# Optimization experiments

Measured on AMD Instinct MI355X. Metric: run time of the kernel, lower is better.

## Reference

```python
import jax, jax.numpy as jnp
import numpy as np

B, N, K, C = 8, 4096, 32, 64
RADIUS = 0.15
CIN = C + 3  # dp_fj: concat(dp[3], fj[C])


def _ball_query(p, radius, k):
    """p: (B,N,3). Returns neighbor indices (B,N,K): first k points (in index
    order) within radius of each query, padded with the first valid neighbor
    (ballquery semantics; query point itself is always index 0 candidate)."""
    sq = jnp.sum(p * p, axis=-1)                                  # (B,N)
    d2 = sq[:, :, None] + sq[:, None, :] - 2.0 * jnp.einsum('bnd,bmd->bnm', p, p)
    n = p.shape[1]
    within = d2 <= radius * radius
    key = jnp.where(within, jnp.arange(n, dtype=jnp.int32)[None, None, :], n)
    order = jnp.argsort(key, axis=-1)[..., :k]                    # (B,N,K)
    valid = jnp.take_along_axis(key, order, axis=-1) < n
    first = order[..., :1]
    return jnp.where(valid, order, first)


def _conv2d_1x1(x, w, b):
    # x: (B,Cin,N,K), w: (Cout,Cin), b: (Cout,)
    return jnp.einsum('oi,bink->bonk', w, x) + b[None, :, None, None]


def _conv1d_1x1(x, w, b):
    # x: (B,Cin,N)
    return jnp.einsum('oi,bin->bon', w, x) + b[None, :, None]


def setup_inputs() -> dict:
    key = jax.random.key(0)
    ks = jax.random.split(key, 16)
    s = 0.05
    inp = {
        'p': jax.random.uniform(ks[0], (B, N, 3), dtype=jnp.float32),
        'f': jax.random.normal(ks[1], (B, C, N), dtype=jnp.float32),
        # attn_local: convblock2d (CIN -> C), no act
        'w_attn': jax.random.normal(ks[2], (C, CIN), dtype=jnp.float32) * s,
        'b_attn': jnp.zeros((C,), jnp.float32),
        # convs: convblock2d (CIN -> C, relu) then (C -> C, no act)
        'w1': jax.random.normal(ks[3], (C, CIN), dtype=jnp.float32) * s,
        'b1': jnp.zeros((C,), jnp.float32),
        'w2': jax.random.normal(ks[4], (C, C), dtype=jnp.float32) * s,
        'b2': jnp.zeros((C,), jnp.float32),
        # ffn: convblock1d (C -> C*expansion=C, relu) then (C -> C, no act)
        'wf1': jax.random.normal(ks[5], (C, C), dtype=jnp.float32) * s,
        'bf1': jnp.zeros((C,), jnp.float32),
        'wf2': jax.random.normal(ks[6], (C, C), dtype=jnp.float32) * s,
        'bf2': jnp.zeros((C,), jnp.float32),
    }
    return inp


def reference(p, f, w_attn, b_attn, w1, b1, w2, b2, wf1, bf1, wf2, bf2):
    bidx = jnp.arange(B)[:, None, None]
    idx = _ball_query(p, RADIUS, K)                               # (B,N,K) int
    pj = p[bidx, idx]                                             # (B,N,K,3)
    dp = (pj - p[:, :, None, :]).transpose(0, 3, 1, 2)            # (B,3,N,K)
    ft = f.transpose(0, 2, 1)                                     # (B,N,C)
    fj = ft[bidx, idx].transpose(0, 3, 1, 2)                      # (B,C,N,K)

    fj_cat = jnp.concatenate([dp, fj], axis=1)                    # (B,CIN,N,K)

    attn = _conv2d_1x1(fj_cat, w_attn, b_attn)                    # (B,C,N,K)
    x = jax.nn.relu(_conv2d_1x1(fj_cat, w1, b1))
    x = _conv2d_1x1(x, w2, b2)                                    # (B,C,N,K)

    # new_attention, 4D path: softmax over neighbor axis (tau=1), weighted sum
    channel_attn = jax.nn.softmax(attn, axis=-1)
    fout = jnp.sum(channel_attn * x, axis=-1)                     # (B,C,N)

    fout = jax.nn.relu(fout + f)
    identity = fout
    h = jax.nn.relu(_conv1d_1x1(fout, wf1, bf1))
    h = _conv1d_1x1(h, wf2, bf2)
    fout = jax.nn.relu(h + identity)                              # use_res
    return (p, fout)
```

## Files before the change

kernel.cpp:

```cpp
#include <hip/hip_runtime.h>

#define B_ 8
#define N_ 4096
#define K_ 32
#define C_ 64
#define CIN_ 67
#define R2_ 0.0225f

#define SFJ 104
#define SY1 72
#define SFB 72
#define PTS 4
#define ITERS 4

typedef short short8v __attribute__((ext_vector_type(8)));
typedef short short4v __attribute__((ext_vector_type(4)));
typedef float floatx4 __attribute__((ext_vector_type(4)));

__device__ __forceinline__ short f2bf(float x) {
    unsigned u = __float_as_uint(x);
    u += 0x7fffu + ((u >> 16) & 1u);
    return (short)(u >> 16);
}

__global__ __launch_bounds__(256) void prep_kernel(
    const float* __restrict__ p, const float* __restrict__ f,
    unsigned short* __restrict__ ftb, float4* __restrict__ p4,
    float* __restrict__ pout)
{
#pragma clang fp contract(off)
    __shared__ short tile[64 * 72];
    const int t = threadIdx.x;
    const int b = blockIdx.x >> 6;
    const int n0 = (blockIdx.x & 63) * 64;
    const int nn4 = t & 15, ch = t >> 4;
    for (int cc = 0; cc < 4; ++cc) {
        const int c = cc * 16 + ch;
        const float4 v = *(const float4*)&f[((size_t)(b * 64 + c)) * N_ + n0 + nn4 * 4];
        tile[(nn4 * 4 + 0) * 72 + c] = f2bf(v.x);
        tile[(nn4 * 4 + 1) * 72 + c] = f2bf(v.y);
        tile[(nn4 * 4 + 2) * 72 + c] = f2bf(v.z);
        tile[(nn4 * 4 + 3) * 72 + c] = f2bf(v.w);
    }
    if (t < 48) {
        const size_t base = ((size_t)(b * N_ + n0)) * 3;
        ((float4*)(pout + base))[t] = ((const float4*)(p + base))[t];
    }
    if (t < 64) {
        const int n = n0 + t;
        const float x = p[((size_t)(b * N_ + n)) * 3 + 0];
        const float y = p[((size_t)(b * N_ + n)) * 3 + 1];
        const float z = p[((size_t)(b * N_ + n)) * 3 + 2];
        const float sq = (x * x + y * y) + z * z;
        p4[(size_t)b * N_ + n] = make_float4(x, y, z, sq);
    }
    __syncthreads();
    const int nn = t >> 2, cb = (t & 3) * 16;
    uint4* dst = (uint4*)&ftb[((size_t)(b * N_ + n0 + nn)) * 64 + cb];
    const uint4* src = (const uint4*)&tile[nn * 72 + cb];
    dst[0] = src[0];
    dst[1] = src[1];
}

__global__ __launch_bounds__(256) void ball_query_kernel(
    const float4* __restrict__ p4, unsigned short* __restrict__ idx)
{
#pragma clang fp contract(off)
    const int lane = threadIdx.x & 63;
    const int q = (blockIdx.x * blockDim.x + threadIdx.x) >> 6;
    const int b = q >> 12;
    const int n = q & (N_ - 1);
    const float4* pb = p4 + (size_t)b * N_;
    const float4 Q = pb[n];
    unsigned short* out = idx + (size_t)q * K_;
    int count = 0;
    int first = -1;
    for (int base = 0; base < N_; base += 128) {
        const float4 A  = pb[base + lane];
        const float4 Bv = pb[base + 64 + lane];
        const float d2a = (Q.w + A.w)  - 2.0f * ((Q.x * A.x  + Q.y * A.y)  + Q.z * A.z);
        const float d2b = (Q.w + Bv.w) - 2.0f * ((Q.x * Bv.x + Q.y * Bv.y) + Q.z * Bv.z);
        const bool wa = d2a <= R2_;
        const bool wb = d2b <= R2_;
        const unsigned long long m0 = __ballot(wa);
        const unsigned long long m1 = __ballot(wb);
        if (m0 | m1) {
            if (first < 0)
                first = m0 ? (base + __builtin_ctzll(m0))
                           : (base + 64 + __builtin_ctzll(m1));
            const int c0 = __popcll(m0);
            const unsigned long long below = (1ull << lane) - 1ull;
            if (wa) {
                const int pos = count + __popcll(m0 & below);
                if (pos < K_) out[pos] = (unsigned short)(base + lane);
            }
            if (wb) {
                const int pos = count + c0 + __popcll(m1 & below);
                if (pos < K_) out[pos] = (unsigned short)(base + 64 + lane);
            }
            count += c0 + __popcll(m1);
            if (count >= K_) break;
        }
    }
    for (int pos = count + lane; pos < K_; pos += 64) out[pos] = (unsigned short)first;
}

__global__ __launch_bounds__(256, 3) void lpa_mfma_kernel(
    const float4* __restrict__ p4, const float* __restrict__ f,
    const unsigned short* __restrict__ ftb,
    const float* __restrict__ w_attn, const float* __restrict__ b_attn,
    const float* __restrict__ w1, const float* __restrict__ b1,
    const float* __restrict__ w2, const float* __restrict__ b2,
    const float* __restrict__ wf1, const float* __restrict__ bf1,
    const float* __restrict__ wf2, const float* __restrict__ bf2,
    const unsigned short* __restrict__ idx, float* __restrict__ out)
{
    __shared__ __align__(16) short s_fj[128 * SFJ];
    __shared__ __align__(16) short s_y1[128 * SY1];
    __shared__ __align__(16) short s_fbuf[2 * 16 * SFB];
    __shared__ float s_vec[PTS * 64];
    short* s_vecbf = s_fbuf;
    short* s_hbf   = s_fbuf + 16 * SFB;

    const int t = threadIdx.x;
    const int lane = t & 63;
    const int mb = t >> 6;
    const int l15 = lane & 15;
    const int quad = lane >> 4;

    short8v wa_f[3], w1_f[3], w2_f[2], wf1_f[2], wf2_f[2];
    {
        const int cm = mb * 16 + l15;
        #pragma unroll
        for (int ks = 0; ks < 3; ++ks) {
            short8v a, bq;
            #pragma unroll
            for (int j = 0; j < 8; ++j) {
                const int ip = ks * 32 + quad * 8 + j;
                float va = 0.0f, vb = 0.0f;
                if (ip < 64)      { va = w_attn[cm * CIN_ + ip + 3];  vb = w1[cm * CIN_ + ip + 3]; }
                else if (ip < 67) { va = w_attn[cm * CIN_ + ip - 64]; vb = w1[cm * CIN_ + ip - 64]; }
                a[j] = f2bf(va); bq[j] = f2bf(vb);
            }
            wa_f[ks] = a; w1_f[ks] = bq;
        }
        #pragma unroll
        for (int ks = 0; ks < 2; ++ks) {
            short8v a, bq, cq;
            #pragma unroll
            for (int j = 0; j < 8; ++j) {
                const int kk = ks * 32 + quad * 8 + j;
                a[j]  = f2bf(w2[cm * 64 + kk]);
                bq[j] = f2bf(wf1[cm * 64 + kk]);
                cq[j] = f2bf(wf2[cm * 64 + kk]);
            }
            w2_f[ks] = a; wf1_f[ks] = bq; wf2_f[ks] = cq;
        }
    }

    const int crow = mb * 16 + quad * 4;
    const float4 bav  = *(const float4*)&b_attn[crow];
    const float4 b1v  = *(const float4*)&b1[crow];
    const float4 b2v  = *(const float4*)&b2[crow];
    const float4 bf1v = *(const float4*)&bf1[crow];
    const float4 bf2v = *(const float4*)&bf2[crow];

    for (int e = t; e < 512; e += 256) {
        const int col = e >> 2, c4 = e & 3;
        *(uint4*)&s_fj[col * SFJ + 72 + c4 * 8] = make_uint4(0u, 0u, 0u, 0u);
    }
    for (int e = t; e < 1152; e += 256) ((unsigned*)s_fbuf)[e] = 0u;

    const int pt00 = blockIdx.x * (PTS * ITERS);
    for (int itn = 0; itn < ITERS; ++itn) {
        const int pt0 = pt00 + itn * PTS;
        const int b = pt0 >> 12;

        {
            const int col = t >> 1, h = t & 1;
            const int j = idx[pt0 * K_ + col];
            const uint4* src = (const uint4*)&ftb[((size_t)(b * N_ + j)) * 64 + h * 32];
            uint4* dst = (uint4*)&s_fj[col * SFJ + h * 32];
            dst[0] = src[0]; dst[1] = src[1]; dst[2] = src[2]; dst[3] = src[3];
            if (h) {
                const int n = (pt0 + (col >> 5)) & (N_ - 1);
                const float4 Pj = p4[(size_t)b * N_ + j];
                const float4 Pn = p4[(size_t)b * N_ + n];
                short8v dp = {};
                dp[0] = f2bf(Pj.x - Pn.x);
                dp[1] = f2bf(Pj.y - Pn.y);
                dp[2] = f2bf(Pj.z - Pn.z);
                *(short8v*)&s_fj[col * SFJ + 64] = dp;
            }
        }
        __syncthreads();

        floatx4 accA[8];
        #pragma unroll
        for (int nt = 0; nt < 8; ++nt) {
            const short* bp = &s_fj[(nt * 16 + l15) * SFJ + quad * 8];
            const short8v fb0 = *(const short8v*)(bp);
            const short8v fb1 = *(const short8v*)(bp + 32);
            const short8v fb2 = *(const short8v*)(bp + 64);
            floatx4 a = {0.f, 0.f, 0.f, 0.f};
            a = __builtin_amdgcn_mfma_f32_16x16x32_bf16(wa_f[0], fb0, a, 0, 0, 0);
            a = __builtin_amdgcn_mfma_f32_16x16x32_bf16(wa_f[1], fb1, a, 0, 0, 0);
            a = __builtin_amdgcn_mfma_f32_16x16x32_bf16(wa_f[2], fb2, a, 0, 0, 0);
            accA[nt] = a;
            floatx4 y = {0.f, 0.f, 0.f, 0.f};
            y = __builtin_amdgcn_mfma_f32_16x16x32_bf16(w1_f[0], fb0, y, 0, 0, 0);
            y = __builtin_amdgcn_mfma_f32_16x16x32_bf16(w1_f[1], fb1, y, 0, 0, 0);
            y = __builtin_amdgcn_mfma_f32_16x16x32_bf16(w1_f[2], fb2, y, 0, 0, 0);
            short4v yp;
            yp[0] = f2bf(fmaxf(y[0] + b1v.x, 0.f));
            yp[1] = f2bf(fmaxf(y[1] + b1v.y, 0.f));
            yp[2] = f2bf(fmaxf(y[2] + b1v.z, 0.f));
            yp[3] = f2bf(fmaxf(y[3] + b1v.w, 0.f));
            *(short4v*)&s_y1[(nt * 16 + l15) * SY1 + crow] = yp;
        }
        __syncthreads();

        floatx4 accX[8];
        #pragma unroll
        for (int nt = 0; nt < 8; ++nt) {
            const short* bp = &s_y1[(nt * 16 + l15) * SY1 + quad * 8];
            const short8v yb0 = *(const short8v*)(bp);
            const short8v yb1 = *(const short8v*)(bp + 32);
            floatx4 x = {0.f, 0.f, 0.f, 0.f};
            x = __builtin_amdgcn_mfma_f32_16x16x32_bf16(w2_f[0], yb0, x, 0, 0, 0);
            x = __builtin_amdgcn_mfma_f32_16x16x32_bf16(w2_f[1], yb1, x, 0, 0, 0);
            accX[nt] = x;
        }

        #pragma unroll
        for (int pi = 0; pi < PTS; ++pi) {
            const int n = (pt0 + pi) & (N_ - 1);
            float fo[4];
            #pragma unroll
            for (int r = 0; r < 4; ++r) {
                const float ba = (r == 0) ? bav.x : (r == 1) ? bav.y : (r == 2) ? bav.z : bav.w;
                const float bx = (r == 0) ? b2v.x : (r == 1) ? b2v.y : (r == 2) ? b2v.z : b2v.w;
                const float va = accA[2 * pi][r] + ba;
                const float vb = accA[2 * pi + 1][r] + ba;
                const float e0 = __expf(va);
                const float e1 = __expf(vb);
                float se = e0 + e1;
                float sw = e0 * (accX[2 * pi][r] + bx) + e1 * (accX[2 * pi + 1][r] + bx);
                se += __shfl_xor(se, 1); sw += __shfl_xor(sw, 1);
                se += __shfl_xor(se, 2); sw += __shfl_xor(sw, 2);
                se += __shfl_xor(se, 4); sw += __shfl_xor(sw, 4);
                se += __shfl_xor(se, 8); sw += __shfl_xor(sw, 8);
                const float fres = f[((size_t)(b * 64 + crow + r)) * N_ + n];
                fo[r] = fmaxf(sw / se + fres, 0.f);
            }
            if (l15 == 0) {
                *(float4*)&s_vec[pi * 64 + crow] = make_float4(fo[0], fo[1], fo[2], fo[3]);
                short4v fb;
                fb[0] = f2bf(fo[0]); fb[1] = f2bf(fo[1]);
                fb[2] = f2bf(fo[2]); fb[3] = f2bf(fo[3]);
                *(short4v*)&s_vecbf[pi * SFB + crow] = fb;
            }
        }
        __syncthreads();

        {
            const short8v vb0 = *(const short8v*)&s_vecbf[l15 * SFB + quad * 8];
            const short8v vb1 = *(const short8v*)&s_vecbf[l15 * SFB + 32 + quad * 8];
            floatx4 d = {0.f, 0.f, 0.f, 0.f};
            d = __builtin_amdgcn_mfma_f32_16x16x32_bf16(wf1_f[0], vb0, d, 0, 0, 0);
            d = __builtin_amdgcn_mfma_f32_16x16x32_bf16(wf1_f[1], vb1, d, 0, 0, 0);
            if (l15 < PTS) {
                short4v hb;
                hb[0] = f2bf(fmaxf(d[0] + bf1v.x, 0.f));
                hb[1] = f2bf(fmaxf(d[1] + bf1v.y, 0.f));
                hb[2] = f2bf(fmaxf(d[2] + bf1v.z, 0.f));
                hb[3] = f2bf(fmaxf(d[3] + bf1v.w, 0.f));
                *(short4v*)&s_hbf[l15 * SFB + crow] = hb;
            }
        }
        __syncthreads();

        {
            const short8v hb0 = *(const short8v*)&s_hbf[l15 * SFB + quad * 8];
            const short8v hb1 = *(const short8v*)&s_hbf[l15 * SFB + 32 + quad * 8];
            floatx4 d = {0.f, 0.f, 0.f, 0.f};
            d = __builtin_amdgcn_mfma_f32_16x16x32_bf16(wf2_f[0], hb0, d, 0, 0, 0);
            d = __builtin_amdgcn_mfma_f32_16x16x32_bf16(wf2_f[1], hb1, d, 0, 0, 0);
            if (l15 < PTS) {
                const int n = (pt0 + l15) & (N_ - 1);
                out[((size_t)(b * 64 + crow + 0)) * N_ + n] =
                    fmaxf(d[0] + bf2v.x + s_vec[l15 * 64 + crow + 0], 0.f);
                out[((size_t)(b * 64 + crow + 1)) * N_ + n] =
                    fmaxf(d[1] + bf2v.y + s_vec[l15 * 64 + crow + 1], 0.f);
                out[((size_t)(b * 64 + crow + 2)) * N_ + n] =
                    fmaxf(d[2] + bf2v.z + s_vec[l15 * 64 + crow + 2], 0.f);
                out[((size_t)(b * 64 + crow + 3)) * N_ + n] =
                    fmaxf(d[3] + bf2v.w + s_vec[l15 * 64 + crow + 3], 0.f);
            }
        }
    }
}

extern "C" void kernel_launch(void* const* d_in, const int* in_sizes, int n_in,
                              void* d_out, int out_size, void* d_ws, size_t ws_size,
                              hipStream_t stream)
{
    const float* p      = (const float*)d_in[0];
    const float* f      = (const float*)d_in[1];
    const float* w_attn = (const float*)d_in[2];
    const float* b_attn = (const float*)d_in[3];
    const float* w1     = (const float*)d_in[4];
    const float* b1     = (const float*)d_in[5];
    const float* w2     = (const float*)d_in[6];
    const float* b2     = (const float*)d_in[7];
    const float* wf1    = (const float*)d_in[8];
    const float* bf1    = (const float*)d_in[9];
    const float* wf2    = (const float*)d_in[10];
    const float* bf2    = (const float*)d_in[11];
    float* out = (float*)d_out;

    unsigned short* idx = (unsigned short*)d_ws;
    unsigned short* ftb = (unsigned short*)((char*)d_ws + 2u * 1024 * 1024);
    float4* p4          = (float4*)((char*)d_ws + 6u * 1024 * 1024);

    prep_kernel<<<B_ * (N_ / 64), 256, 0, stream>>>(p, f, ftb, p4, out);
    ball_query_kernel<<<(B_ * N_) / 4, 256, 0, stream>>>(p4, idx);
    lpa_mfma_kernel<<<(B_ * N_) / (PTS * ITERS), 256, 0, stream>>>(
        p4, f, ftb, w_attn, b_attn, w1, b1, w2, b2, wf1, bf1, wf2, bf2,
        idx, out + (size_t)B_ * N_ * 3);
}
```

Measured before the change: 264.8 us.

## Fuse ball query into the MFMA kernel, keeping neighbor indices in LDS

Removes the separate ball_query kernel. Each wave of the main kernel now runs the neighbor search for 4 query points at once, sharing each candidate point load across those queries, and writes the indices into shared memory instead of a global buffer. This drops one launch and the global round trip of the index array. The scan loop only exits once all 4 queries have 32 neighbors, so a wave can do more iterations than before. The softmax division is also replaced with a fast reciprocal.

```diff
diff --git a/kernel.cpp b/kernel.cpp
--- a/kernel.cpp
+++ b/kernel.cpp
@@ -62,50 +62,7 @@
     dst[1] = src[1];
 }
 
-__global__ __launch_bounds__(256) void ball_query_kernel(
-    const float4* __restrict__ p4, unsigned short* __restrict__ idx)
-{
-#pragma clang fp contract(off)
-    const int lane = threadIdx.x & 63;
-    const int q = (blockIdx.x * blockDim.x + threadIdx.x) >> 6;
-    const int b = q >> 12;
-    const int n = q & (N_ - 1);
-    const float4* pb = p4 + (size_t)b * N_;
-    const float4 Q = pb[n];
-    unsigned short* out = idx + (size_t)q * K_;
-    int count = 0;
-    int first = -1;
-    for (int base = 0; base < N_; base += 128) {
-        const float4 A  = pb[base + lane];
-        const float4 Bv = pb[base + 64 + lane];
-        const float d2a = (Q.w + A.w)  - 2.0f * ((Q.x * A.x  + Q.y * A.y)  + Q.z * A.z);
-        const float d2b = (Q.w + Bv.w) - 2.0f * ((Q.x * Bv.x + Q.y * Bv.y) + Q.z * Bv.z);
-        const bool wa = d2a <= R2_;
-        const bool wb = d2b <= R2_;
-        const unsigned long long m0 = __ballot(wa);
-        const unsigned long long m1 = __ballot(wb);
-        if (m0 | m1) {
-            if (first < 0)
-                first = m0 ? (base + __builtin_ctzll(m0))
-                           : (base + 64 + __builtin_ctzll(m1));
-            const int c0 = __popcll(m0);
-            const unsigned long long below = (1ull << lane) - 1ull;
-            if (wa) {
-                const int pos = count + __popcll(m0 & below);
-                if (pos < K_) out[pos] = (unsigned short)(base + lane);
-            }
-            if (wb) {
-                const int pos = count + c0 + __popcll(m1 & below);
-                if (pos < K_) out[pos] = (unsigned short)(base + 64 + lane);
-            }
-            count += c0 + __popcll(m1);
-            if (count >= K_) break;
-        }
-    }
-    for (int pos = count + lane; pos < K_; pos += 64) out[pos] = (unsigned short)first;
-}
-
-__global__ __launch_bounds__(256, 3) void lpa_mfma_kernel(
+__global__ __launch_bounds__(256, 3) void lpa_mega_kernel(
     const float4* __restrict__ p4, const float* __restrict__ f,
     const unsigned short* __restrict__ ftb,
     const float* __restrict__ w_attn, const float* __restrict__ b_attn,
@@ -113,12 +70,13 @@
     const float* __restrict__ w2, const float* __restrict__ b2,
     const float* __restrict__ wf1, const float* __restrict__ bf1,
     const float* __restrict__ wf2, const float* __restrict__ bf2,
-    const unsigned short* __restrict__ idx, float* __restrict__ out)
+    float* __restrict__ out)
 {
     __shared__ __align__(16) short s_fj[128 * SFJ];
     __shared__ __align__(16) short s_y1[128 * SY1];
     __shared__ __align__(16) short s_fbuf[2 * 16 * SFB];
     __shared__ float s_vec[PTS * 64];
+    __shared__ unsigned short s_idx[16 * K_];
     short* s_vecbf = s_fbuf;
     short* s_hbf   = s_fbuf + 16 * SFB;
 
@@ -127,6 +85,57 @@
     const int mb = t >> 6;
     const int l15 = lane & 15;
     const int quad = lane >> 4;
+
+    const int blk_pt0 = blockIdx.x * (PTS * ITERS);
+    const int bb = blk_pt0 >> 12;
+    const float4* pb = p4 + (size_t)bb * N_;
+
+    for (int e = t; e < 512; e += 256) {
+        const int col = e >> 2, c4 = e & 3;
+        *(uint4*)&s_fj[col * SFJ + 72 + c4 * 8] = make_uint4(0u, 0u, 0u, 0u);
+    }
+    for (int e = t; e < 1152; e += 256) ((unsigned*)s_fbuf)[e] = 0u;
+
+    {
+#pragma clang fp contract(off)
+        float4 Q[4];
+        #pragma unroll
+        for (int q = 0; q < 4; ++q)
+            Q[q] = pb[(blk_pt0 + mb * 4 + q) & (N_ - 1)];
+        int count[4] = {0, 0, 0, 0};
+        int first[4] = {-1, -1, -1, -1};
+        for (int base = 0; base < N_; base += 64) {
+            const float4 A = pb[base + lane];
+            unsigned long long m[4];
+            bool w[4];
+            #pragma unroll
+            for (int q = 0; q < 4; ++q) {
+                const float d2 = (Q[q].w + A.w)
+                    - 2.0f * ((Q[q].x * A.x + Q[q].y * A.y) + Q[q].z * A.z);
+                w[q] = (d2 <= R2_);
+                m[q] = __ballot(w[q]);
+            }
+            const unsigned long long below = (1ull << lane) - 1ull;
+            #pragma unroll
+            for (int q = 0; q < 4; ++q) {
+                if (m[q]) {
+                    if (first[q] < 0) first[q] = base + __builtin_ctzll(m[q]);
+                    if (w[q]) {
+                        const int pos = count[q] + __popcll(m[q] & below);
+                        if (pos < K_)
+                            s_idx[(mb * 4 + q) * K_ + pos] = (unsigned short)(base + lane);
+                    }
+                    count[q] += __popcll(m[q]);
+                }
+            }
+            if (count[0] >= K_ && count[1] >= K_ && count[2] >= K_ && count[3] >= K_)
+                break;
+        }
+        #pragma unroll
+        for (int q = 0; q < 4; ++q)
+            for (int pos = count[q] + lane; pos < K_; pos += 64)
+                s_idx[(mb * 4 + q) * K_ + pos] = (unsigned short)first[q];
+    }
 
     short8v wa_f[3], w1_f[3], w2_f[2], wf1_f[2], wf2_f[2];
     {
@@ -165,27 +174,21 @@
     const float4 bf1v = *(const float4*)&bf1[crow];
     const float4 bf2v = *(const float4*)&bf2[crow];
 
-    for (int e = t; e < 512; e += 256) {
-        const int col = e >> 2, c4 = e & 3;
-        *(uint4*)&s_fj[col * SFJ + 72 + c4 * 8] = make_uint4(0u, 0u, 0u, 0u);
-    }
-    for (int e = t; e < 1152; e += 256) ((unsigned*)s_fbuf)[e] = 0u;
-
-    const int pt00 = blockIdx.x * (PTS * ITERS);
+    __syncthreads();
+
     for (int itn = 0; itn < ITERS; ++itn) {
-        const int pt0 = pt00 + itn * PTS;
-        const int b = pt0 >> 12;
+        const int pt0 = blk_pt0 + itn * PTS;
 
         {
             const int col = t >> 1, h = t & 1;
-            const int j = idx[pt0 * K_ + col];
-            const uint4* src = (const uint4*)&ftb[((size_t)(b * N_ + j)) * 64 + h * 32];
+            const int j = s_idx[itn * 128 + col];
+            const uint4* src = (const uint4*)&ftb[((size_t)(bb * N_ + j)) * 64 + h * 32];
             uint4* dst = (uint4*)&s_fj[col * SFJ + h * 32];
             dst[0] = src[0]; dst[1] = src[1]; dst[2] = src[2]; dst[3] = src[3];
             if (h) {
                 const int n = (pt0 + (col >> 5)) & (N_ - 1);
-                const float4 Pj = p4[(size_t)b * N_ + j];
-                const float4 Pn = p4[(size_t)b * N_ + n];
+                const float4 Pj = pb[j];
+                const float4 Pn = pb[n];
                 short8v dp = {};
                 dp[0] = f2bf(Pj.x - Pn.x);
                 dp[1] = f2bf(Pj.y - Pn.y);
@@ -250,8 +253,8 @@
                 se += __shfl_xor(se, 2); sw += __shfl_xor(sw, 2);
                 se += __shfl_xor(se, 4); sw += __shfl_xor(sw, 4);
                 se += __shfl_xor(se, 8); sw += __shfl_xor(sw, 8);
-                const float fres = f[((size_t)(b * 64 + crow + r)) * N_ + n];
-                fo[r] = fmaxf(sw / se + fres, 0.f);
+                const float fres = f[((size_t)(bb * 64 + crow + r)) * N_ + n];
+                fo[r] = fmaxf(sw * __builtin_amdgcn_rcpf(se) + fres, 0.f);
             }
             if (l15 == 0) {
                 *(float4*)&s_vec[pi * 64 + crow] = make_float4(fo[0], fo[1], fo[2], fo[3]);
@@ -288,13 +291,13 @@
             d = __builtin_amdgcn_mfma_f32_16x16x32_bf16(wf2_f[1], hb1, d, 0, 0, 0);
             if (l15 < PTS) {
                 const int n = (pt0 + l15) & (N_ - 1);
-                out[((size_t)(b * 64 + crow + 0)) * N_ + n] =
+                out[((size_t)(bb * 64 + crow + 0)) * N_ + n] =
                     fmaxf(d[0] + bf2v.x + s_vec[l15 * 64 + crow + 0], 0.f);
-                out[((size_t)(b * 64 + crow + 1)) * N_ + n] =
+                out[((size_t)(bb * 64 + crow + 1)) * N_ + n] =
                     fmaxf(d[1] + bf2v.y + s_vec[l15 * 64 + crow + 1], 0.f);
-                out[((size_t)(b * 64 + crow + 2)) * N_ + n] =
+                out[((size_t)(bb * 64 + crow + 2)) * N_ + n] =
                     fmaxf(d[2] + bf2v.z + s_vec[l15 * 64 + crow + 2], 0.f);
-                out[((size_t)(b * 64 + crow + 3)) * N_ + n] =
+                out[((size_t)(bb * 64 + crow + 3)) * N_ + n] =
                     fmaxf(d[3] + bf2v.w + s_vec[l15 * 64 + crow + 3], 0.f);
             }
         }
@@ -319,13 +322,11 @@
     const float* bf2    = (const float*)d_in[11];
     float* out = (float*)d_out;
 
-    unsigned short* idx = (unsigned short*)d_ws;
-    unsigned short* ftb = (unsigned short*)((char*)d_ws + 2u * 1024 * 1024);
-    float4* p4          = (float4*)((char*)d_ws + 6u * 1024 * 1024);
+    unsigned short* ftb = (unsigned short*)d_ws;
+    float4* p4          = (float4*)((char*)d_ws + 4u * 1024 * 1024);
 
     prep_kernel<<<B_ * (N_ / 64), 256, 0, stream>>>(p, f, ftb, p4, out);
-    ball_query_kernel<<<(B_ * N_) / 4, 256, 0, stream>>>(p4, idx);
-    lpa_mfma_kernel<<<(B_ * N_) / (PTS * ITERS), 256, 0, stream>>>(
+    lpa_mega_kernel<<<(B_ * N_) / (PTS * ITERS), 256, 0, stream>>>(
         p4, f, ftb, w_attn, b_attn, w1, b1, w2, b2, wf1, bf1, wf2, bf2,
-        idx, out + (size_t)B_ * N_ * 3);
+        out + (size_t)B_ * N_ * 3);
 }
```

Result: slower. 281.3 us (+6.2%).
